# Performance work log

Hardware: AMD Instinct MI355X
Metric: run time of the kernel (lower is better)

The kernel has to match this reference:

```python
import jax, jax.numpy as jnp
import numpy as np

N, E = 10000, 100000
WIDTH, KER_WIDTH, DEPTH = 32, 128, 3
EDGE_ATTR_DIM, IN_WIDTH, OUT_WIDTH, COORD_DIM = 6, 3, 1, 3


def _glorot(k, fan_in, fan_out):
    return jax.random.normal(k, (fan_in, fan_out), jnp.float32) / np.sqrt(fan_in).astype(np.float32)


def setup_inputs() -> dict:
    key = jax.random.key(0)
    ks = jax.random.split(key, 16)
    z = lambda n: jnp.zeros((n,), jnp.float32)
    return {
        "x": jax.random.normal(ks[0], (N, IN_WIDTH), jnp.float32),
        "edge_index": jax.random.randint(ks[1], (2, E), 0, N),
        "edge_attr": jax.random.normal(ks[2], (E, EDGE_ATTR_DIM), jnp.float32),
        "coords_init": jax.random.normal(ks[3], (N, COORD_DIM), jnp.float32),
        "fc1_w": _glorot(ks[4], IN_WIDTH, WIDTH), "fc1_b": z(WIDTH),
        "ker_w1": _glorot(ks[5], EDGE_ATTR_DIM + 1, KER_WIDTH // 2), "ker_b1": z(KER_WIDTH // 2),
        "ker_w2": _glorot(ks[6], KER_WIDTH // 2, KER_WIDTH), "ker_b2": z(KER_WIDTH),
        "ker_w3": _glorot(ks[7], KER_WIDTH, WIDTH * WIDTH), "ker_b3": z(WIDTH * WIDTH),
        "cm_w1": _glorot(ks[8], WIDTH, WIDTH), "cm_b1": z(WIDTH),
        "cm_w2": _glorot(ks[9], WIDTH, 1) * 1e-3,  # xavier gain=0.001 coord head, no bias
        "fc2_w1": _glorot(ks[10], WIDTH, 2 * WIDTH), "fc2_b1": z(2 * WIDTH),
        "fc2_w2": _glorot(ks[11], 2 * WIDTH, OUT_WIDTH), "fc2_b2": z(OUT_WIDTH),
    }


def _seg_mean(data, seg, n):
    s = jax.ops.segment_sum(data, seg, num_segments=n)
    c = jax.ops.segment_sum(jnp.ones((seg.shape[0], 1), data.dtype), seg, num_segments=n)
    return s / jnp.clip(c, 1.0)


def reference(x, edge_index, edge_attr, coords_init,
              fc1_w, fc1_b, ker_w1, ker_b1, ker_w2, ker_b2, ker_w3, ker_b3,
              cm_w1, cm_b1, cm_w2, fc2_w1, fc2_b1, fc2_w2, fc2_b2):
    row, col = edge_index[0], edge_index[1]
    h = x @ fc1_w + fc1_b                                   # [N, W]
    coord = coords_init
    for _ in range(DEPTH):
        coord_diff = coord[row] - coord[col]                # [E, 3]
        radial = jnp.sum(coord_diff * coord_diff, axis=-1, keepdims=True)
        kin = jnp.concatenate([edge_attr, radial], axis=-1)  # [E, ker_in]
        k = jax.nn.relu(kin @ ker_w1 + ker_b1)
        k = jax.nn.relu(k @ ker_w2 + ker_b2)
        Wk = (k @ ker_w3 + ker_b3).reshape(E, WIDTH, WIDTH)  # per-edge kernel matrix
        m = jnp.einsum('eij,ej->ei', Wk, h[col])             # per-edge message [E, W]
        phi = jax.nn.relu(m @ cm_w1 + cm_b1) @ cm_w2         # [E, 1]
        coord = coord + _seg_mean(coord_diff * phi, row, N)  # equivariant coord update
        h = jax.nn.relu(h + _seg_mean(m, row, N))            # GKN node update
    out = jax.nn.relu(h @ fc2_w1 + fc2_b1) @ fc2_w2 + fc2_b2  # [N, out_width]
    return out, coord
```

## Files before the change

kernel.cpp:

```cpp
#include <hip/hip_runtime.h>
#include <hip/hip_bf16.h>

#define NN 10000
#define NE 100000
#define NSEG_MAX 16384

typedef __bf16 bf16x8 __attribute__((ext_vector_type(8)));
typedef float  f32x4  __attribute__((ext_vector_type(4)));

__device__ __forceinline__ f32x4 relu4(f32x4 a) {
    a.x = fmaxf(a.x, 0.f); a.y = fmaxf(a.y, 0.f);
    a.z = fmaxf(a.z, 0.f); a.w = fmaxf(a.w, 0.f);
    return a;
}

__device__ __forceinline__ unsigned pk2(float a, float b) {
    unsigned ua = (unsigned)__builtin_bit_cast(unsigned short, (__bf16)a);
    unsigned ub = (unsigned)__builtin_bit_cast(unsigned short, (__bf16)b);
    return ua | (ub << 16);
}

__global__ void k_setup(const float* __restrict__ w3, __bf16* __restrict__ w3t_sw,
                        const float* __restrict__ b3, __bf16* __restrict__ b3t_sw,
                        const float* __restrict__ w2, __bf16* __restrict__ w2t_sw,
                        const float* __restrict__ cw1, __bf16* __restrict__ cmw1_sw,
                        const float* __restrict__ x, const float* __restrict__ fc1w,
                        const float* __restrict__ fc1b, const float* __restrict__ cinit,
                        float* __restrict__ h, float* __restrict__ coord,
                        const int* __restrict__ eidx,
                        int* __restrict__ deg, int* __restrict__ within,
                        int* __restrict__ degc, int* __restrict__ withinc) {
    int t = blockIdx.x * blockDim.x + threadIdx.x;
    if (t < 131072) {
        int jj = t & 7, l = (t >> 3) & 63, ut = t >> 9;
        int u  = ut*16 + (l & 15);
        int j2 = ((l >> 4) & 3)*8 + jj;
        int f  = u >> 9, ll = (u >> 3) & 63, j0 = u & 7;
        int c  = (f & 3)*32 + ((ll >> 4) & 3)*8 + j0;
        int i  = (f >> 2)*16 + (ll & 15);
        w3t_sw[t] = (__bf16)w3[c*1024 + i*32 + j2];
    } else if (t < 132096) {
        int idx = t - 131072;
        int jj = idx & 7, l = (idx >> 3) & 63, tt = idx >> 9;
        int i  = tt*16 + (l & 15);
        int j2 = ((l >> 4) & 3)*8 + jj;
        b3t_sw[idx] = (__bf16)b3[i*32 + j2];
    } else if (t < 140288) {
        int idx = t - 132096;
        int jj = idx & 7, l = (idx >> 3) & 63, g = idx >> 9;
        int ct = g >> 1, ks = g & 1;
        int c  = ct*16 + (l & 15);
        int ch = ks*32 + ((l >> 4) & 3)*8 + jj;
        w2t_sw[idx] = (__bf16)w2[ch*128 + c];
    } else if (t < 142336) {
        int idx = t - 140288;
        int jj = idx & 7, l = (idx >> 3) & 63, ot = idx >> 9;
        int o  = ot*16 + (l & 15);
        int i  = ((l >> 4) & 3)*8 + jj;
        cmw1_sw[idx] = (__bf16)cw1[i*32 + o];
    } else if (t < 142336 + NN) {
        int n = t - 142336;
        float x0 = x[n*3+0], x1 = x[n*3+1], x2 = x[n*3+2];
        #pragma unroll
        for (int j = 0; j < 32; j += 4) {
            f32x4 a = *(const f32x4*)(fc1b + j);
            a += x0 * (*(const f32x4*)(fc1w + 0*32 + j));
            a += x1 * (*(const f32x4*)(fc1w + 1*32 + j));
            a += x2 * (*(const f32x4*)(fc1w + 2*32 + j));
            *(f32x4*)(h + n*32 + j) = a;
        }
        coord[n*3+0] = cinit[n*3+0];
        coord[n*3+1] = cinit[n*3+1];
        coord[n*3+2] = cinit[n*3+2];
    } else if (t < 142336 + NN + NE) {
        int e = t - 142336 - NN;
        within[e] = atomicAdd(&deg[eidx[e]], 1);
    } else if (t < 142336 + NN + 2*NE) {
        int e = t - 142336 - NN - NE;
        withinc[e] = atomicAdd(&degc[eidx[NE + e]], 1);
    }
}

__global__ __launch_bounds__(1024, 1)
void k_scan(const int* __restrict__ deg, int* __restrict__ rowptr,
            float* __restrict__ deg_inv,
            const int* __restrict__ degc, int* __restrict__ colptr,
            int* __restrict__ seg_meta, int* __restrict__ seg_start) {
    __shared__ int s0a[1024], s1a[1024], s2a[1024];
    const int tid = threadIdx.x;
    const int CH = 10;
    const int base = tid * CH;

    int a = 0, b = 0, c = 0;
    for (int i = 0; i < CH; ++i) {
        int n = base + i;
        if (n < NN) {
            int d0 = deg[n], d1 = degc[n];
            a += d0; b += d1; c += (d1 + 15) >> 4;
        }
    }
    s0a[tid] = a; s1a[tid] = b; s2a[tid] = c;
    __syncthreads();
    for (int off = 1; off < 1024; off <<= 1) {
        int t0 = (tid >= off) ? s0a[tid - off] : 0;
        int t1 = (tid >= off) ? s1a[tid - off] : 0;
        int t2 = (tid >= off) ? s2a[tid - off] : 0;
        __syncthreads();
        s0a[tid] += t0; s1a[tid] += t1; s2a[tid] += t2;
        __syncthreads();
    }
    int run0 = s0a[tid] - a;
    int run1 = s1a[tid] - b;
    int run2 = s2a[tid] - c;
    for (int i = 0; i < CH; ++i) {
        int n = base + i;
        if (n < NN) {
            int d0 = deg[n];
            rowptr[n] = run0; run0 += d0;
            deg_inv[n] = 1.0f / (float)(d0 > 1 ? d0 : 1);
            int d1 = degc[n];
            colptr[n] = run1;
            int ns = (d1 + 15) >> 4;
            for (int k = 0; k < ns; ++k) {
                int cnt = d1 - k*16; if (cnt > 16) cnt = 16;
                seg_meta[run2 + k]  = n | (cnt << 16);
                seg_start[run2 + k] = run1 + k*16;
            }
            run1 += d1; run2 += ns;
        }
    }
    if (tid == 1023) { rowptr[NN] = s0a[1023]; colptr[NN] = s1a[1023]; }
    __syncthreads();
    int nseg = s2a[1023];
    for (int sg = nseg + tid; sg < NSEG_MAX; sg += 1024) {
        seg_meta[sg] = -1;
        seg_start[sg] = 0;
    }
}

__global__ void k_setup2(const int* __restrict__ eidx, const float* __restrict__ eattr,
                         const int* __restrict__ rowptr, const int* __restrict__ within,
                         const int* __restrict__ colptr, const int* __restrict__ withinc,
                         int* __restrict__ cs_pos, int* __restrict__ cs_row,
                         float* __restrict__ eattr_cs) {
    int e = blockIdx.x * blockDim.x + threadIdx.x;
    if (e >= NE) return;
    int row = eidx[e], col = eidx[NE + e];
    int pos = rowptr[row] + within[e];
    int cs  = colptr[col] + withinc[e];
    cs_pos[cs] = pos; cs_row[cs] = row;
    #pragma unroll
    for (int a = 0; a < 6; ++a) eattr_cs[(size_t)cs*8 + a] = eattr[(size_t)e*6 + a];
    eattr_cs[(size_t)cs*8 + 6] = 0.f; eattr_cs[(size_t)cs*8 + 7] = 0.f;
}

__global__ __launch_bounds__(1024, 4)
void k_edge(const int* __restrict__ seg_meta, const int* __restrict__ seg_start,
            const int* __restrict__ cs_pos, const int* __restrict__ cs_row,
            const float* __restrict__ eattr_cs, const float* __restrict__ coord,
            const float* __restrict__ w1, const float* __restrict__ b1,
            const __bf16* __restrict__ w2t_sw, const float* __restrict__ b2,
            const __bf16* __restrict__ w3t_sw, const __bf16* __restrict__ b3t_sw,
            const float* __restrict__ h,
            const __bf16* __restrict__ cmw1_sw, const float* __restrict__ cm_b1,
            const float* __restrict__ cm_w2,
            float* __restrict__ cds, float* __restrict__ m_s,
            float* __restrict__ phis) {
    __shared__ __align__(16) __bf16 r_lds[16 * 2048];
    __shared__ __align__(16) __bf16 wlds[10240];
    const int tid  = threadIdx.x;
    const int lane = tid & 63;
    const int wave = tid >> 6;
    const int q  = lane >> 4;
    const int el = lane & 15;
    const int sb = blockIdx.x * 16;
    if (seg_meta[sb] < 0) return;

    {
        ((f32x4*)wlds)[tid] = ((const f32x4*)w2t_sw)[tid];
        if (tid < 256) ((f32x4*)(wlds + 8192))[tid] = ((const f32x4*)cmw1_sw)[tid];
    }

    const int mown = seg_meta[sb + wave];
    const bool live = mown >= 0;
    const int v_own = live ? (mown & 0xFFFF) : 0;
    const int cnt   = mown >> 16;
    int start = seg_start[sb + wave];

    const int mel = seg_meta[sb + el];
    const int vel = (mel < 0) ? 0 : (mel & 0xFFFF);
    bf16x8 bfrag;
    {
        const float* hp = h + (size_t)vel * 32 + q * 8;
        f32x4 h0 = *(const f32x4*)hp;
        f32x4 h1 = *(const f32x4*)(hp + 4);
        bfrag[0]=(__bf16)h0.x; bfrag[1]=(__bf16)h0.y; bfrag[2]=(__bf16)h0.z; bfrag[3]=(__bf16)h0.w;
        bfrag[4]=(__bf16)h1.x; bfrag[5]=(__bf16)h1.y; bfrag[6]=(__bf16)h1.z; bfrag[7]=(__bf16)h1.w;
    }

    int slot = start + el; if (slot >= NE) slot = NE - 1;
    const int pos   = cs_pos[slot];
    const int rnode = cs_row[slot];
    const float dx = coord[rnode*3+0] - coord[v_own*3+0];
    const float dy = coord[rnode*3+1] - coord[v_own*3+1];
    const float dz = coord[rnode*3+2] - coord[v_own*3+2];
    const float rad = dx*dx + dy*dy + dz*dz;
    f32x4 ea0 = *(const f32x4*)(eattr_cs + (size_t)slot*8);
    f32x4 ea1 = *(const f32x4*)(eattr_cs + (size_t)slot*8 + 4);
    const float kin[7] = {ea0.x, ea0.y, ea0.z, ea0.w, ea1.x, ea1.y, rad};

    const f32x4 zero = {0.f, 0.f, 0.f, 0.f};

    auto phaseA = [&](int halfsel) {
        #pragma unroll
        for (int s = 0; s < 8; ++s) {
            const int idx = wave*8 + s;
            const int fh = idx >> 5, g = idx & 31;
            const int f  = ((fh & 1) | ((fh & 2) << 1)) + halfsel*2;
            const int ut = f*32 + g;
            bf16x8 af = *(const bf16x8*)(w3t_sw + ((size_t)ut*64 + lane)*8);
            f32x4 c = __builtin_amdgcn_mfma_f32_16x16x32_bf16(af, bfrag, zero, 0, 0, 0);
            const int wb = el*4096 + ((fh*1024 + g*32 + q*8) ^ ((el & 7) << 4));
            *(uint2*)((char*)r_lds + wb) = make_uint2(pk2(c.x, c.y), pk2(c.z, c.w));
        }
    };

    phaseA(0);

    bf16x8 k1f[2];
    #pragma unroll
    for (int ks = 0; ks < 2; ++ks) {
        const int c0 = ks*32 + q*8;
        f32x4 a0 = *(const f32x4*)(b1 + c0);
        f32x4 a1 = *(const f32x4*)(b1 + c0 + 4);
        #pragma unroll
        for (int a = 0; a < 7; ++a) {
            const float kv = kin[a];
            a0 += kv * (*(const f32x4*)(w1 + a*64 + c0));
            a1 += kv * (*(const f32x4*)(w1 + a*64 + c0 + 4));
        }
        a0 = relu4(a0); a1 = relu4(a1);
        bf16x8 t;
        t[0]=(__bf16)a0.x; t[1]=(__bf16)a0.y; t[2]=(__bf16)a0.z; t[3]=(__bf16)a0.w;
        t[4]=(__bf16)a1.x; t[5]=(__bf16)a1.y; t[6]=(__bf16)a1.z; t[7]=(__bf16)a1.w;
        k1f[ks] = t;
    }

    __syncthreads();

    f32x4 C2[8];
    #pragma unroll
    for (int ct = 0; ct < 8; ++ct) {
        f32x4 acc = zero;
        #pragma unroll
        for (int ks = 0; ks < 2; ++ks) {
            bf16x8 af = *(const bf16x8*)(wlds + ((ct*2 + ks)*64 + lane)*8);
            acc = __builtin_amdgcn_mfma_f32_16x16x32_bf16(af, k1f[ks], acc, 0, 0, 0);
        }
        f32x4 bb = *(const f32x4*)(b2 + ct*16 + q*4);
        C2[ct] = relu4(acc + bb);
    }

    const int lowq = q & 1, hiq = q >> 1;
    bf16x8 k2f[4];
    #pragma unroll
    for (int ks2 = 0; ks2 < 4; ++ks2) {
        bf16x8 t;
        #pragma unroll
        for (int hh = 0; hh < 2; ++hh) {
            const int src = (lowq*2 + hh)*16 + el;
            #pragma unroll
            for (int rr = 0; rr < 4; ++rr) {
                const float x0 = __shfl(C2[ks2*2][rr],     src, 64);
                const float x1 = __shfl(C2[ks2*2 + 1][rr], src, 64);
                t[hh*4 + rr] = (__bf16)(hiq ? x1 : x0);
            }
        }
        k2f[ks2] = t;
    }

    f32x4 M0 = zero, M1 = zero;
    auto mhalf = [&](int k2lo) {
        bf16x8 rA[4];
        #pragma unroll
        for (int fh = 0; fh < 4; ++fh) {
            const int rb = wave*4096 + ((fh*1024 + lane*16) ^ ((wave & 7) << 4));
            rA[fh] = *(const bf16x8*)((const char*)r_lds + rb);
        }
        M0 = __builtin_amdgcn_mfma_f32_16x16x32_bf16(rA[0], k2f[k2lo],   M0, 0, 0, 0);
        M0 = __builtin_amdgcn_mfma_f32_16x16x32_bf16(rA[1], k2f[k2lo+1], M0, 0, 0, 0);
        M1 = __builtin_amdgcn_mfma_f32_16x16x32_bf16(rA[2], k2f[k2lo],   M1, 0, 0, 0);
        M1 = __builtin_amdgcn_mfma_f32_16x16x32_bf16(rA[3], k2f[k2lo+1], M1, 0, 0, 0);
    };

    mhalf(0);
    __syncthreads();
    phaseA(1);
    __syncthreads();
    mhalf(2);

    {
        bf16x8 a0 = *(const bf16x8*)(b3t_sw + ((size_t)0*64 + lane)*8);
        bf16x8 a1 = *(const bf16x8*)(b3t_sw + ((size_t)1*64 + lane)*8);
        f32x4 bt0 = __builtin_amdgcn_mfma_f32_16x16x32_bf16(a0, bfrag, zero, 0, 0, 0);
        f32x4 bt1 = __builtin_amdgcn_mfma_f32_16x16x32_bf16(a1, bfrag, zero, 0, 0, 0);
        f32x4 btv0, btv1;
        #pragma unroll
        for (int r = 0; r < 4; ++r) {
            btv0[r] = __shfl(bt0[r], (lane & 48) + wave, 64);
            btv1[r] = __shfl(bt1[r], (lane & 48) + wave, 64);
        }
        M0 += btv0; M1 += btv1;
    }

    const bool ev = live && (el < cnt);
    if (ev) {
        *(f32x4*)(m_s + (size_t)pos*32 + q*4)      = M0;
        *(f32x4*)(m_s + (size_t)pos*32 + 16 + q*4) = M1;
        if (q == 0) {
            f32x4 cdv = {dx, dy, dz, rad};
            *(f32x4*)(cds + (size_t)pos*4) = cdv;
        }
    }

    bf16x8 paf;
    #pragma unroll
    for (int hh = 0; hh < 2; ++hh) {
        const int src = (lowq*2 + hh)*16 + el;
        #pragma unroll
        for (int rr = 0; rr < 4; ++rr) {
            const float x0 = __shfl(M0[rr], src, 64);
            const float x1 = __shfl(M1[rr], src, 64);
            paf[hh*4 + rr] = (__bf16)(hiq ? x1 : x0);
        }
    }
    bf16x8 bf0 = *(const bf16x8*)(wlds + 8192 + (0*64 + lane)*8);
    bf16x8 bf1 = *(const bf16x8*)(wlds + 8192 + (1*64 + lane)*8);
    f32x4 PH0 = __builtin_amdgcn_mfma_f32_16x16x32_bf16(paf, bf0, zero, 0, 0, 0);
    f32x4 PH1 = __builtin_amdgcn_mfma_f32_16x16x32_bf16(paf, bf1, zero, 0, 0, 0);

    const float b1v0 = cm_b1[el], b1v1 = cm_b1[16 + el];
    const float w2v0 = cm_w2[el], w2v1 = cm_w2[16 + el];
    float ph[4]; int pr[4];
    #pragma unroll
    for (int r = 0; r < 4; ++r) {
        float s0 = fmaxf(PH0[r] + b1v0, 0.f) * w2v0
                 + fmaxf(PH1[r] + b1v1, 0.f) * w2v1;
        s0 += __shfl_xor(s0, 1, 64);
        s0 += __shfl_xor(s0, 2, 64);
        s0 += __shfl_xor(s0, 4, 64);
        s0 += __shfl_xor(s0, 8, 64);
        ph[r] = s0;
        pr[r] = __shfl(pos, (q << 4) + q*4 + r, 64);
    }
    if (live && el == 0) {
        #pragma unroll
        for (int r = 0; r < 4; ++r)
            if (q*4 + r < cnt) phis[pr[r]] = ph[r];
    }
}

__global__ __launch_bounds__(256, 4)
void k_gather(const int* __restrict__ rowptr,
              const float* __restrict__ m_s, const float* __restrict__ phis,
              const float* __restrict__ cds, const float* __restrict__ deg_inv,
              float* __restrict__ coord, float* __restrict__ h,
              const float* __restrict__ fw1, const float* __restrict__ fb1,
              const float* __restrict__ fw2, const float* __restrict__ fb2,
              float* __restrict__ out, int dofinal) {
    int tid = blockIdx.x * blockDim.x + threadIdx.x;
    int n = tid >> 3, sub = tid & 7;
    if (n >= NN) return;
    int st = rowptr[n], en = rowptr[n+1];
    f32x4 am0 = {0.f, 0.f, 0.f, 0.f}, am1 = {0.f, 0.f, 0.f, 0.f};
    f32x4 am2 = {0.f, 0.f, 0.f, 0.f}, am3 = {0.f, 0.f, 0.f, 0.f};
    int p = st;
    for (; p + 3 < en; p += 4) {
        am0 += *(const f32x4*)(m_s + (size_t)p*32 + sub*4);
        am1 += *(const f32x4*)(m_s + (size_t)(p+1)*32 + sub*4);
        am2 += *(const f32x4*)(m_s + (size_t)(p+2)*32 + sub*4);
        am3 += *(const f32x4*)(m_s + (size_t)(p+3)*32 + sub*4);
    }
    for (; p < en; ++p)
        am0 += *(const f32x4*)(m_s + (size_t)p*32 + sub*4);
    f32x4 am = (am0 + am1) + (am2 + am3);

    float di = deg_inv[n];
    f32x4 hv = *(const f32x4*)(h + (size_t)n*32 + sub*4);
    hv = relu4(hv + am * di);

    float cx = 0.f, cy = 0.f, cz = 0.f;
    for (int pp = st + sub; pp < en; pp += 8) {
        f32x4 cd = *(const f32x4*)(cds + (size_t)pp*4);
        float ph = phis[pp];
        cx += cd.x * ph; cy += cd.y * ph; cz += cd.z * ph;
    }
    cx += __shfl_xor(cx, 1, 64); cy += __shfl_xor(cy, 1, 64); cz += __shfl_xor(cz, 1, 64);
    cx += __shfl_xor(cx, 2, 64); cy += __shfl_xor(cy, 2, 64); cz += __shfl_xor(cz, 2, 64);
    cx += __shfl_xor(cx, 4, 64); cy += __shfl_xor(cy, 4, 64); cz += __shfl_xor(cz, 4, 64);
    float c0 = 0.f, c1 = 0.f, c2 = 0.f;
    if (sub == 0) {
        c0 = coord[n*3+0] + cx * di;
        c1 = coord[n*3+1] + cy * di;
        c2 = coord[n*3+2] + cz * di;
    }

    if (!dofinal) {
        *(f32x4*)(h + (size_t)n*32 + sub*4) = hv;
        if (sub == 0) {
            coord[n*3+0] = c0; coord[n*3+1] = c1; coord[n*3+2] = c2;
        }
        return;
    }

    const int gbase = (tid & 63) & 56;
    float hreg[32];
    #pragma unroll
    for (int s2 = 0; s2 < 8; ++s2) {
        hreg[s2*4+0] = __shfl(hv.x, gbase + s2, 64);
        hreg[s2*4+1] = __shfl(hv.y, gbase + s2, 64);
        hreg[s2*4+2] = __shfl(hv.z, gbase + s2, 64);
        hreg[s2*4+3] = __shfl(hv.w, gbase + s2, 64);
    }
    float po = 0.f;
    #pragma unroll
    for (int oo = 0; oo < 8; oo += 4) {
        int o = sub*8 + oo;
        f32x4 a = *(const f32x4*)(fb1 + o);
        #pragma unroll
        for (int i = 0; i < 32; ++i)
            a += hreg[i] * (*(const f32x4*)(fw1 + i*64 + o));
        a = relu4(a);
        f32x4 w2 = *(const f32x4*)(fw2 + o);
        po += a.x*w2.x + a.y*w2.y + a.z*w2.z + a.w*w2.w;
    }
    po += __shfl_xor(po, 1, 64);
    po += __shfl_xor(po, 2, 64);
    po += __shfl_xor(po, 4, 64);
    if (sub == 0) {
        out[n] = po + fb2[0];
        out[NN + n*3 + 0] = c0;
        out[NN + n*3 + 1] = c1;
        out[NN + n*3 + 2] = c2;
    }
}


extern "C" void kernel_launch(void* const* d_in, const int* in_sizes, int n_in,
                              void* d_out, int out_size, void* d_ws, size_t ws_size,
                              hipStream_t stream) {
    const float* x      = (const float*)d_in[0];
    const int*   eidx   = (const int*)  d_in[1];
    const float* eattr  = (const float*)d_in[2];
    const float* cinit  = (const float*)d_in[3];
    const float* fc1w   = (const float*)d_in[4];
    const float* fc1b   = (const float*)d_in[5];
    const float* kw1    = (const float*)d_in[6];
    const float* kb1    = (const float*)d_in[7];
    const float* kw2    = (const float*)d_in[8];
    const float* kb2    = (const float*)d_in[9];
    const float* kw3    = (const float*)d_in[10];
    const float* kb3    = (const float*)d_in[11];
    const float* cmw1   = (const float*)d_in[12];
    const float* cmb1   = (const float*)d_in[13];
    const float* cmw2   = (const float*)d_in[14];
    const float* f2w1   = (const float*)d_in[15];
    const float* f2b1   = (const float*)d_in[16];
    const float* f2w2   = (const float*)d_in[17];
    const float* f2b2   = (const float*)d_in[18];
    float* out = (float*)d_out;

    char* p = (char*)d_ws;
    auto carve = [&](size_t bytes) {
        void* r = (void*)p;
        p += (bytes + 255) & ~(size_t)255;
        return r;
    };
    float*  h        = (float*) carve((size_t)NN * 32 * 4);
    float*  coord    = (float*) carve((size_t)NN * 3 * 4);
    int*    deg      = (int*)   carve((size_t)NN * 4);
    float*  deg_inv  = (float*) carve((size_t)NN * 4);
    int*    rowptr   = (int*)   carve((size_t)(NN + 1) * 4);
    int*    within   = (int*)   carve((size_t)NE * 4);
    int*    degc     = (int*)   carve((size_t)NN * 4);
    int*    colptr   = (int*)   carve((size_t)(NN + 1) * 4);
    int*    withinc  = (int*)   carve((size_t)NE * 4);
    int*    cs_pos   = (int*)   carve((size_t)NE * 4);
    int*    cs_row   = (int*)   carve((size_t)NE * 4);
    float*  eattr_cs = (float*) carve((size_t)NE * 8 * 4);
    int*    seg_meta = (int*)   carve((size_t)NSEG_MAX * 4);
    int*    seg_start= (int*)   carve((size_t)NSEG_MAX * 4);
    float*  cds      = (float*) carve((size_t)NE * 4 * 4);
    float*  m_s      = (float*) carve((size_t)NE * 32 * 4);
    float*  phis     = (float*) carve((size_t)NE * 4);
    __bf16* w3t_sw   = (__bf16*)carve((size_t)131072 * 2);
    __bf16* b3t_sw   = (__bf16*)carve((size_t)1024 * 2);
    __bf16* w2t_sw   = (__bf16*)carve((size_t)8192 * 2);
    __bf16* cmw1_sw  = (__bf16*)carve((size_t)2048 * 2);

    const int TB = 256;
    dim3 b(TB);
    const int totS = 142336 + NN + 2*NE;
    dim3 gS((totS + TB - 1) / TB);
    dim3 gS2((NE + TB - 1) / TB);
    dim3 gE(NSEG_MAX / 16);
    dim3 gA((NN*8 + TB - 1) / TB);

    hipMemsetAsync(deg, 0, (size_t)NN * 4, stream);
    hipMemsetAsync(degc, 0, (size_t)NN * 4, stream);
    k_setup<<<gS, b, 0, stream>>>(kw3, w3t_sw, kb3, b3t_sw, kw2, w2t_sw, cmw1, cmw1_sw,
                                  x, fc1w, fc1b, cinit, h, coord, eidx,
                                  deg, within, degc, withinc);
    k_scan<<<1, dim3(1024), 0, stream>>>(deg, rowptr, deg_inv, degc, colptr,
                                         seg_meta, seg_start);
    k_setup2<<<gS2, b, 0, stream>>>(eidx, eattr, rowptr, within, colptr, withinc,
                                    cs_pos, cs_row, eattr_cs);

    for (int d = 0; d < 3; ++d) {
        k_edge<<<gE, dim3(1024), 0, stream>>>(seg_meta, seg_start, cs_pos, cs_row,
                                              eattr_cs, coord, kw1, kb1, w2t_sw, kb2,
                                              w3t_sw, b3t_sw, h, cmw1_sw, cmb1, cmw2,
                                              cds, m_s, phis);
        k_gather<<<gA, b, 0, stream>>>(rowptr, m_s, phis, cds, deg_inv, coord, h,
                                       f2w1, f2b1, f2w2, f2b2, out, d == 2 ? 1 : 0);
    }
}
```

Before: 311.8 us.

## Double LDS staging buffer to compute full per-edge kernel in one pass

```diff
diff --git a/kernel.cpp b/kernel.cpp
--- a/kernel.cpp
+++ b/kernel.cpp
@@ -166,7 +166,7 @@
             const float* __restrict__ cm_w2,
             float* __restrict__ cds, float* __restrict__ m_s,
             float* __restrict__ phis) {
-    __shared__ __align__(16) __bf16 r_lds[16 * 2048];
+    __shared__ __align__(16) __bf16 r_lds[16 * 4096];
     __shared__ __align__(16) __bf16 wlds[10240];
     const int tid  = threadIdx.x;
     const int lane = tid & 63;
@@ -211,21 +211,17 @@
 
     const f32x4 zero = {0.f, 0.f, 0.f, 0.f};
 
-    auto phaseA = [&](int halfsel) {
-        #pragma unroll
-        for (int s = 0; s < 8; ++s) {
-            const int idx = wave*8 + s;
-            const int fh = idx >> 5, g = idx & 31;
-            const int f  = ((fh & 1) | ((fh & 2) << 1)) + halfsel*2;
-            const int ut = f*32 + g;
-            bf16x8 af = *(const bf16x8*)(w3t_sw + ((size_t)ut*64 + lane)*8);
+    {
+        #pragma unroll
+        for (int s = 0; s < 16; ++s) {
+            const int idx = wave*16 + s;
+            const int f = idx >> 5, g = idx & 31;
+            bf16x8 af = *(const bf16x8*)(w3t_sw + ((size_t)(f*32 + g)*64 + lane)*8);
             f32x4 c = __builtin_amdgcn_mfma_f32_16x16x32_bf16(af, bfrag, zero, 0, 0, 0);
-            const int wb = el*4096 + ((fh*1024 + g*32 + q*8) ^ ((el & 7) << 4));
+            const int wb = el*8192 + ((f*1024 + g*32 + q*8) ^ ((el & 7) << 4));
             *(uint2*)((char*)r_lds + wb) = make_uint2(pk2(c.x, c.y), pk2(c.z, c.w));
         }
-    };
-
-    phaseA(0);
+    }
 
     bf16x8 k1f[2];
     #pragma unroll
@@ -280,24 +276,13 @@
     }
 
     f32x4 M0 = zero, M1 = zero;
-    auto mhalf = [&](int k2lo) {
-        bf16x8 rA[4];
-        #pragma unroll
-        for (int fh = 0; fh < 4; ++fh) {
-            const int rb = wave*4096 + ((fh*1024 + lane*16) ^ ((wave & 7) << 4));
-            rA[fh] = *(const bf16x8*)((const char*)r_lds + rb);
-        }
-        M0 = __builtin_amdgcn_mfma_f32_16x16x32_bf16(rA[0], k2f[k2lo],   M0, 0, 0, 0);
-        M0 = __builtin_amdgcn_mfma_f32_16x16x32_bf16(rA[1], k2f[k2lo+1], M0, 0, 0, 0);
-        M1 = __builtin_amdgcn_mfma_f32_16x16x32_bf16(rA[2], k2f[k2lo],   M1, 0, 0, 0);
-        M1 = __builtin_amdgcn_mfma_f32_16x16x32_bf16(rA[3], k2f[k2lo+1], M1, 0, 0, 0);
-    };
-
-    mhalf(0);
-    __syncthreads();
-    phaseA(1);
-    __syncthreads();
-    mhalf(2);
+    #pragma unroll
+    for (int f = 0; f < 8; ++f) {
+        const int rb = wave*8192 + ((f*1024 + lane*16) ^ ((wave & 7) << 4));
+        bf16x8 rA = *(const bf16x8*)((const char*)r_lds + rb);
+        if (f < 4) M0 = __builtin_amdgcn_mfma_f32_16x16x32_bf16(rA, k2f[f & 3], M0, 0, 0, 0);
+        else       M1 = __builtin_amdgcn_mfma_f32_16x16x32_bf16(rA, k2f[f & 3], M1, 0, 0, 0);
+    }
 
     {
         bf16x8 a0 = *(const bf16x8*)(b3t_sw + ((size_t)0*64 + lane)*8);
```

After: 301.6 us. -3.3%, faster.
